# Optimization experiments

Hardware: AMD Instinct MI355X
Metric: run time of the kernel (lower is better)

The kernel has to match this reference:

```python
import jax, jax.numpy as jnp
import numpy as np

TEMPERATURE = 0.07
DELTA = 0.3
KA = 2.0
R = 3
B = 4096
D = 512
K = 4096
N = 131072
N_DICT_KEYS = 3  # len(cluster_result) dict: inst2cluster/centroids/density


def _l2norm(x):
    # torch F.normalize: x / max(||x||, 1e-12)
    return x / jnp.maximum(jnp.linalg.norm(x, axis=-1, keepdims=True), 1e-12)


def _inst_inst(anchor, pos):
    # CE with label 0 on [diag, off-diag] == logsumexp(full row) - diag
    a = _l2norm(anchor)
    p = _l2norm(pos)
    logits = (a @ p.T) / TEMPERATURE  # [B, B]
    return jax.nn.logsumexp(logits, axis=1) - jnp.diagonal(logits)


def _off_diag_idx(b):
    # row i -> column indices [0..b-1] excluding i (row-major boolean-mask order)
    j = jnp.arange(b - 1)[None, :]
    return j + (j >= jnp.arange(b)[:, None]).astype(jnp.int32)


def _inst_proto(anchor, i2c, centroids, density, index):
    b = anchor.shape[0]
    a = _l2norm(anchor)
    oidx = _off_diag_idx(b)
    loss = jnp.zeros(b, dtype=anchor.dtype)
    for r in range(R):
        protos = _l2norm(centroids[r])           # [K, D]
        pid = i2c[r][index]                       # [B]
        sim = a @ protos[pid].T                   # [B, B]
        diag = jnp.diagonal(sim)
        off = jnp.take_along_axis(sim, oidx, axis=1)  # [B, B-1]
        # faithful to original: divide concatenated logits column-wise by density[pid]
        logits = jnp.concatenate([diag[:, None], off], axis=1) / density[r][pid][None, :]
        loss = loss + (jax.nn.logsumexp(logits, axis=1) - logits[:, 0])
        loss = loss / N_DICT_KEYS  # original divides INSIDE the loop
    return loss


def _weights(audio, frame, a_i2c, a_cent, f_i2c, f_cent, index):
    fa = _l2norm(audio)
    ff = _l2norm(frame)
    rho = jnp.sum(fa * ff, axis=1)  # diagonal of fa @ ff.T
    for r in range(R):
        ca = a_cent[r][a_i2c[r][index]]  # [B, D] (NOT normalized, as in original)
        cf = f_cent[r][f_i2c[r][index]]
        rho = rho - jnp.sum(ca * cf, axis=1)  # diagonal of ca @ cf.T
    order = jnp.argsort(rho)
    sorted_rho = rho[order]
    mu = rho.mean() + DELTA * rho.std()
    sigma = rho.std() * jnp.sqrt(jnp.asarray(KA, rho.dtype))
    y = jnp.exp(-0.5 * ((sorted_rho - mu) / sigma) ** 2) / (jnp.sqrt(2.0 * jnp.pi) * sigma)
    y = jnp.cumsum(y)
    y = y / y[-1]
    w = y[jnp.argsort(order)]  # y at the rank of each rho_i
    return jax.lax.stop_gradient(w)  # original detaches via cpu().numpy()


def _forward(audio_emb, frame_emb, a_centroids, a_density, f_centroids, f_density,
             video_index, a_inst2cluster, f_inst2cluster):
    loss_v2f_ii = _inst_inst(audio_emb, frame_emb)
    loss_f2v_ii = _inst_inst(frame_emb, audio_emb)
    loss_v2f_ip = _inst_proto(audio_emb, f_inst2cluster, f_centroids, f_density, video_index)
    loss_f2v_ip = _inst_proto(frame_emb, a_inst2cluster, a_centroids, a_density, video_index)
    w = _weights(audio_emb, frame_emb, a_inst2cluster, a_centroids,
                 f_inst2cluster, f_centroids, video_index)
    loss_v2f = jnp.sum(w * (loss_v2f_ii + loss_v2f_ip)) / jnp.sum(w)
    loss_f2v = jnp.sum(w * (loss_f2v_ii + loss_f2v_ip)) / jnp.sum(w)
    return loss_v2f + loss_f2v


def setup_inputs() -> dict:
    key = jax.random.key(0)
    ks = jax.random.split(key, 9)
    return {
        "audio_emb": jax.random.normal(ks[0], (B, D), jnp.float32),
        "frame_emb": jax.random.normal(ks[1], (B, D), jnp.float32),
        "a_centroids": jax.random.normal(ks[2], (R, K, D), jnp.float32),
        "a_density": jax.random.uniform(ks[3], (R, K), jnp.float32, 0.3, 1.3),
        "f_centroids": jax.random.normal(ks[4], (R, K, D), jnp.float32),
        "f_density": jax.random.uniform(ks[5], (R, K), jnp.float32, 0.3, 1.3),
        "video_index": jax.random.randint(ks[6], (B,), 0, N),
        "a_inst2cluster": jax.random.randint(ks[7], (R, N), 0, K),
        "f_inst2cluster": jax.random.randint(ks[8], (R, N), 0, K),
    }


def reference(audio_emb, frame_emb, a_centroids, a_density, f_centroids, f_density,
              video_index, a_inst2cluster, f_inst2cluster):
    return _forward(audio_emb, frame_emb, a_centroids, a_density, f_centroids, f_density,
                    video_index, a_inst2cluster, f_inst2cluster)
```

## Files before the change

kernel.cpp:

```cpp
#include <hip/hip_runtime.h>
#include <math.h>

#define B 4096
#define D 512
#define KC 4096
#define NIDX 131072
#define RR 3
#define TEMP 0.07f
#define M_II 14.5f
#define M_IP 4.0f

typedef __bf16 bf16x8 __attribute__((ext_vector_type(8)));
typedef float f32x4 __attribute__((ext_vector_type(4)));

__device__ __forceinline__ void gload_lds16(const void* g, void* l) {
  __builtin_amdgcn_global_load_lds(
      (const __attribute__((address_space(1))) unsigned int*)g,
      (__attribute__((address_space(3))) unsigned int*)l, 16, 0, 0);
}

__device__ __forceinline__ float dot8(float4 a0, float4 a1, float4 b0, float4 b1) {
  return a0.x * b0.x + a0.y * b0.y + a0.z * b0.z + a0.w * b0.w
       + a1.x * b1.x + a1.y * b1.y + a1.z * b1.z + a1.w * b1.w;
}

__global__ __launch_bounds__(256) void prep_kernel(
    const float* __restrict__ audio, const float* __restrict__ frame,
    const float* __restrict__ a_cent, const float* __restrict__ a_dens,
    const float* __restrict__ f_cent, const float* __restrict__ f_dens,
    const int* __restrict__ vidx, const int* __restrict__ a_i2c,
    const int* __restrict__ f_i2c,
    __bf16* __restrict__ Xa, __bf16* __restrict__ Xf,
    __bf16* __restrict__ Yf, __bf16* __restrict__ Ya,
    float* __restrict__ invdd_f, float* __restrict__ invdd_a,
    float* __restrict__ rho0, float* __restrict__ pcp) {
  const int u = blockIdx.x * 4 + (threadIdx.x >> 6);
  const int lane = threadIdx.x & 63;

  if (u < 2 * B) {
    const float* src; __bf16* dst;
    if (u < B) { src = audio + (size_t)u * D; dst = Xa + (size_t)u * D; }
    else       { src = frame + (size_t)(u - B) * D; dst = Xf + (size_t)(u - B) * D; }
    const float4* s4 = (const float4*)src + lane * 2;
    float4 v0 = s4[0], v1 = s4[1];
    float ss = dot8(v0, v1, v0, v1);
    #pragma unroll
    for (int off = 32; off >= 1; off >>= 1) ss += __shfl_xor(ss, off, 64);
    float invn = 1.f / fmaxf(sqrtf(ss), 1e-12f);
    __bf16 o[8];
    o[0] = (__bf16)(v0.x * invn); o[1] = (__bf16)(v0.y * invn);
    o[2] = (__bf16)(v0.z * invn); o[3] = (__bf16)(v0.w * invn);
    o[4] = (__bf16)(v1.x * invn); o[5] = (__bf16)(v1.y * invn);
    o[6] = (__bf16)(v1.z * invn); o[7] = (__bf16)(v1.w * invn);
    *(bf16x8*)(dst + lane * 8) = *(bf16x8*)o;
  } else if (u < 5 * B) {
    const int q = u - 2 * B;
    const int r = q >> 12;
    const int j = q & (B - 1);
    const int idx = vidx[j];
    const int fp = f_i2c[r * NIDX + idx];
    const int ap = a_i2c[r * NIDX + idx];
    const float4* fr4 = (const float4*)(f_cent + ((size_t)r * KC + fp) * D) + lane * 2;
    const float4* ar4 = (const float4*)(a_cent + ((size_t)r * KC + ap) * D) + lane * 2;
    float4 f0 = fr4[0], f1 = fr4[1];
    float4 a0 = ar4[0], a1 = ar4[1];
    float sf = dot8(f0, f1, f0, f1);
    float sa = dot8(a0, a1, a0, a1);
    float pc = dot8(a0, a1, f0, f1);
    #pragma unroll
    for (int off = 32; off >= 1; off >>= 1) {
      sf += __shfl_xor(sf, off, 64);
      sa += __shfl_xor(sa, off, 64);
      pc += __shfl_xor(pc, off, 64);
    }
    float invnf = 1.f / fmaxf(sqrtf(sf), 1e-12f);
    float invna = 1.f / fmaxf(sqrtf(sa), 1e-12f);
    const int slot = r * B + j;
    __bf16 of[8], oa[8];
    of[0] = (__bf16)(f0.x * invnf); of[1] = (__bf16)(f0.y * invnf);
    of[2] = (__bf16)(f0.z * invnf); of[3] = (__bf16)(f0.w * invnf);
    of[4] = (__bf16)(f1.x * invnf); of[5] = (__bf16)(f1.y * invnf);
    of[6] = (__bf16)(f1.z * invnf); of[7] = (__bf16)(f1.w * invnf);
    oa[0] = (__bf16)(a0.x * invna); oa[1] = (__bf16)(a0.y * invna);
    oa[2] = (__bf16)(a0.z * invna); oa[3] = (__bf16)(a0.w * invna);
    oa[4] = (__bf16)(a1.x * invna); oa[5] = (__bf16)(a1.y * invna);
    oa[6] = (__bf16)(a1.z * invna); oa[7] = (__bf16)(a1.w * invna);
    *(bf16x8*)(Yf + (size_t)slot * D + lane * 8) = *(bf16x8*)of;
    *(bf16x8*)(Ya + (size_t)slot * D + lane * 8) = *(bf16x8*)oa;
    if (lane == 0) {
      invdd_f[slot] = 1.f / f_dens[(size_t)r * KC + fp];
      invdd_a[slot] = 1.f / a_dens[(size_t)r * KC + ap];
      pcp[slot] = pc;
    }
  } else {
    const int i = u - 5 * B;
    const float4* x4 = (const float4*)(audio + (size_t)i * D) + lane * 2;
    const float4* y4 = (const float4*)(frame + (size_t)i * D) + lane * 2;
    float4 a0 = x4[0], a1 = x4[1], f0 = y4[0], f1 = y4[1];
    float saf = dot8(a0, a1, f0, f1);
    float sa = dot8(a0, a1, a0, a1);
    float sf = dot8(f0, f1, f0, f1);
    #pragma unroll
    for (int off = 32; off >= 1; off >>= 1) {
      saf += __shfl_xor(saf, off, 64);
      sa  += __shfl_xor(sa, off, 64);
      sf  += __shfl_xor(sf, off, 64);
    }
    if (lane == 0)
      rho0[i] = saf / (fmaxf(sqrtf(sa), 1e-12f) * fmaxf(sqrtf(sf), 1e-12f));
  }
}

__global__ __launch_bounds__(512) void lse_mfma_kernel(
    const __bf16* __restrict__ Xa, const __bf16* __restrict__ Xf,
    const __bf16* __restrict__ Yf, const __bf16* __restrict__ Ya,
    const float* __restrict__ invdd_f, const float* __restrict__ invdd_a,
    float* __restrict__ sp, float* __restrict__ colsp,
    float* __restrict__ diagAll) {
  __shared__ __bf16 As[256 * 32];
  __shared__ __bf16 Bs[256 * 32];
  __shared__ float invL[260];
  __shared__ float part_s[4 * 256];
  __shared__ float colpart[2][256];

  const int b = blockIdx.x;
  const int xcd = b & 7;
  const int bi = b >> 3;
  const int slab = bi >> 4;
  const int w = bi & 15;
  const int gs = xcd * 14 + slab;
  const int yy = gs >> 4;
  const int s = gs & 15;
  const int bx = (s >> 2) * 4 + (w >> 2);
  const int bz = (s & 3) * 4 + (w & 3);

  const int job = (yy == 0) ? 0 : yy + 1;
  const int i0 = bx * 256;
  const int j0 = bz * 256;

  const __bf16* Ab; const __bf16* Bb; const float* invArr = nullptr;
  if (job == 0)      { Ab = Xa; Bb = Xf; }
  else if (job <= 4) { Ab = Xa; Bb = Yf + (size_t)(job - 2) * B * D;
                       invArr = invdd_f + (job - 2) * B; }
  else               { Ab = Xf; Bb = Ya + (size_t)(job - 5) * B * D;
                       invArr = invdd_a + (job - 5) * B; }
  const bool ii = (job == 0);
  const float invT = 1.f / TEMP;
  const float inv0 = ii ? invT : invArr[0];
  const float MJ = ii ? M_II : M_IP;

  const int tid = threadIdx.x;
  const int wv = tid >> 6;
  const int lane = tid & 63;
  const int wr = (wv >> 2) * 128;
  const int wc = (wv & 3) * 64;
  const int g = lane >> 4;
  const int cl = lane & 15;

  if (!ii && tid < 258) {
    int idx = j0 + tid; if (idx > B - 1) idx = B - 1;
    invL[tid] = invArr[idx];
  }

  const int srow = lane >> 2;
  const int skoff = (((lane & 3) ^ ((lane >> 3) & 3)) * 16);
  const int c0row = wv * 16 + srow;
  const char* gA0 = (const char*)Ab + (size_t)(i0 + c0row) * (D * 2) + skoff;
  const char* gA1 = gA0 + (size_t)128 * (D * 2);
  const char* gB0 = (const char*)Bb + (size_t)(j0 + c0row) * (D * 2) + skoff;
  const char* gB1 = gB0 + (size_t)128 * (D * 2);
  __bf16* lA0 = As + wv * 512;
  __bf16* lA1 = As + 4096 + wv * 512;
  __bf16* lB0 = Bs + wv * 512;
  __bf16* lB1 = Bs + 4096 + wv * 512;

  const int csw = (g ^ ((cl >> 1) & 3)) * 8;
  int aoff[8], boff[4];
  #pragma unroll
  for (int t = 0; t < 8; ++t) aoff[t] = (wr + t * 16 + cl) * 32 + csw;
  #pragma unroll
  for (int t = 0; t < 4; ++t) boff[t] = (wc + t * 16 + cl) * 32 + csw;

  f32x4 acc[8][4];
  #pragma unroll
  for (int ri = 0; ri < 8; ++ri)
    #pragma unroll
    for (int ci = 0; ci < 4; ++ci) acc[ri][ci] = (f32x4){0.f, 0.f, 0.f, 0.f};

  for (int kt = 0; kt < 16; ++kt) {
    __syncthreads();
    const int kb = kt * 64;
    gload_lds16(gA0 + kb, lA0);
    gload_lds16(gA1 + kb, lA1);
    gload_lds16(gB0 + kb, lB0);
    gload_lds16(gB1 + kb, lB1);
    __syncthreads();
    bf16x8 af[8], bfr[4];
    #pragma unroll
    for (int t = 0; t < 8; ++t) af[t] = *(const bf16x8*)(As + aoff[t]);
    #pragma unroll
    for (int t = 0; t < 4; ++t) bfr[t] = *(const bf16x8*)(Bs + boff[t]);
    #pragma unroll
    for (int ri = 0; ri < 8; ++ri)
      #pragma unroll
      for (int ci = 0; ci < 4; ++ci)
        acc[ri][ci] = __builtin_amdgcn_mfma_f32_16x16x32_bf16(
            af[ri], bfr[ci], acc[ri][ci], 0, 0, 0);
  }

  const bool dtile = (bx == bz);
  const int co = (j0 < i0) ? 1 : 0;
  float sacc[8][4];
  float csum[4] = {0.f, 0.f, 0.f, 0.f};
  #pragma unroll
  for (int ri = 0; ri < 8; ++ri) {
    #pragma unroll
    for (int v = 0; v < 4; ++v) {
      const int gi = i0 + wr + ri * 16 + g * 4 + v;
      float acc4 = 0.f;
      #pragma unroll
      for (int ci = 0; ci < 4; ++ci) {
        const int jloc = wc + ci * 16 + cl;
        const int gj = j0 + jloc;
        float sc;
        if (ii) sc = invT;
        else if (!dtile) sc = invL[jloc + co];
        else sc = (gj == gi) ? inv0 : invL[(gj < gi) ? (jloc + 1) : jloc];
        float lv = acc[ri][ci][v] * sc;
        if (dtile && gj == gi) diagAll[(size_t)job * B + gi] = lv;
        float ev = __expf(lv - MJ);
        acc4 += ev;
        if (ii) csum[ci] += ev;
      }
      sacc[ri][v] = acc4;
    }
  }
  if (ii) {
    #pragma unroll
    for (int ci = 0; ci < 4; ++ci) {
      csum[ci] += __shfl_xor(csum[ci], 16, 64);
      csum[ci] += __shfl_xor(csum[ci], 32, 64);
    }
    if (g == 0) {
      #pragma unroll
      for (int ci = 0; ci < 4; ++ci)
        colpart[wv >> 2][wc + ci * 16 + cl] = csum[ci];
    }
    __syncthreads();
    if (tid < 256)
      colsp[(size_t)bx * B + j0 + tid] =
          colpart[0][tid] + colpart[1][tid];
  }

  #pragma unroll
  for (int ri = 0; ri < 8; ++ri) {
    #pragma unroll
    for (int v = 0; v < 4; ++v) {
      float s2 = sacc[ri][v];
      #pragma unroll
      for (int off = 8; off >= 1; off >>= 1) s2 += __shfl_xor(s2, off, 64);
      if (cl == 0) part_s[(wv & 3) * 256 + wr + ri * 16 + g * 4 + v] = s2;
    }
  }
  __syncthreads();
  if (tid < 256) {
    size_t o = ((size_t)job * 16 + bz) * B + i0 + tid;
    sp[o] = part_s[tid] + part_s[256 + tid] + part_s[512 + tid] + part_s[768 + tid];
  }
}

__global__ __launch_bounds__(256) void merge_rank_kernel(
    const float* __restrict__ sp, const float* __restrict__ colsp,
    const float* __restrict__ diagAll, const float* __restrict__ rho0,
    const float* __restrict__ pcp,
    float* __restrict__ lossAll, int* __restrict__ rankArr,
    float* __restrict__ srho) {
  __shared__ float lr[B];
  __shared__ float cnt[256];
  const int blk = blockIdx.x;
  const int t = threadIdx.x;
  if (blk < 128) {
    int idx = blk * 256 + t;
    int job = idx >> 12;
    int i = idx & (B - 1);
    if (job == 1) {
      float stot = 0.f;
      #pragma unroll
      for (int x = 0; x < 16; ++x) stot += colsp[(size_t)x * B + i];
      lossAll[idx] = M_II + logf(stot) - diagAll[i];
    } else {
      const float* s16 = sp + (size_t)job * 16 * B + i;
      float stot = 0.f;
      #pragma unroll
      for (int x = 0; x < 16; ++x) stot += s16[(size_t)x * B];
      float MJ = (job < 2) ? M_II : M_IP;
      lossAll[idx] = MJ + logf(stot) - diagAll[(size_t)job * B + i];
    }
  } else {
    const int base = (blk - 128) * 32;
    const int il = t & 31;
    const int i = base + il;
    const int jlo = (t >> 5) * 512;
    for (int k = t; k < B; k += 256)
      lr[k] = rho0[k] - pcp[k] - pcp[B + k] - pcp[2 * B + k];
    __syncthreads();
    float my = lr[i];
    int rk = 0;
    #pragma unroll 8
    for (int j = jlo; j < jlo + 512; ++j) {
      float v = lr[j];
      rk += (v < my) || (v == my && j < i);
    }
    cnt[t] = (float)rk;
    __syncthreads();
    if (t < 32) {
      int r = 0;
      #pragma unroll
      for (int s = 0; s < 8; ++s) r += (int)cnt[s * 32 + t];
      rankArr[i] = r;
      srho[r] = my;
    }
  }
}

__global__ __launch_bounds__(1024) void cdf_final_kernel(
    const float* __restrict__ srho, const int* __restrict__ rankArr,
    const float* __restrict__ lossAll, float* __restrict__ out) {
  __shared__ float pdf[B];
  __shared__ float wred[16], wr1[16], wr2[16];
  __shared__ float wexc[16];
  __shared__ float mv[3];
  const int t = threadIdx.x;
  const int lane = t & 63;
  const int wid = t >> 6;

  float4 sv = *reinterpret_cast<const float4*>(srho + (size_t)t * 4);
  float s = sv.x + sv.y + sv.z + sv.w;
  #pragma unroll
  for (int off = 32; off >= 1; off >>= 1) s += __shfl_xor(s, off, 64);
  if (lane == 0) wred[wid] = s;
  __syncthreads();
  if (t == 0) {
    float tot = 0.f;
    #pragma unroll
    for (int w = 0; w < 16; ++w) tot += wred[w];
    mv[0] = tot / (float)B;
  }
  __syncthreads();
  const float mean = mv[0];
  __syncthreads();
  float dx = sv.x - mean, dy = sv.y - mean, dz = sv.z - mean, dw = sv.w - mean;
  float v = dx * dx + dy * dy + dz * dz + dw * dw;
  #pragma unroll
  for (int off = 32; off >= 1; off >>= 1) v += __shfl_xor(v, off, 64);
  if (lane == 0) wred[wid] = v;
  __syncthreads();
  if (t == 0) {
    float tot = 0.f;
    #pragma unroll
    for (int w = 0; w < 16; ++w) tot += wred[w];
    float sd = sqrtf(tot / (float)B);
    mv[0] = mean + 0.3f * sd;
    mv[1] = sd * 1.41421356237f;
  }
  __syncthreads();
  const float mu = mv[0], sg = mv[1];
  const float c = 1.f / (2.5066282746310002f * sg);
  float p[4];
  {
    float z0 = (sv.x - mu) / sg; p[0] = expf(-0.5f * z0 * z0) * c;
    float z1 = (sv.y - mu) / sg; p[1] = expf(-0.5f * z1 * z1) * c;
    float z2 = (sv.z - mu) / sg; p[2] = expf(-0.5f * z2 * z2) * c;
    float z3 = (sv.w - mu) / sg; p[3] = expf(-0.5f * z3 * z3) * c;
  }
  float chunk = p[0] + p[1] + p[2] + p[3];
  float incl = chunk;
  #pragma unroll
  for (int d = 1; d < 64; d <<= 1) {
    float n = __shfl_up(incl, d, 64);
    if (lane >= d) incl += n;
  }
  if (lane == 63) wred[wid] = incl;
  __syncthreads();
  if (t == 0) {
    float run = 0.f;
    #pragma unroll
    for (int w = 0; w < 16; ++w) { wexc[w] = run; run += wred[w]; }
    mv[2] = run;
  }
  __syncthreads();
  float run = wexc[wid] + (incl - chunk);
  #pragma unroll
  for (int e = 0; e < 4; ++e) { run += p[e]; pdf[t * 4 + e] = run; }
  const float ylast = mv[2];
  __syncthreads();
  int4 rks = *reinterpret_cast<const int4*>(rankArr + (size_t)t * 4);
  float sw = 0.f, s1 = 0.f, s2 = 0.f;
  #pragma unroll
  for (int e = 0; e < 4; ++e) {
    const int i = t * 4 + e;
    const int rk = (e == 0) ? rks.x : (e == 1) ? rks.y : (e == 2) ? rks.z : rks.w;
    float wi = pdf[rk] / ylast;
    float lpv = lossAll[2 * B + i] * (1.f / 27.f) + lossAll[3 * B + i] * (1.f / 9.f)
              + lossAll[4 * B + i] * (1.f / 3.f);
    float lpf = lossAll[5 * B + i] * (1.f / 27.f) + lossAll[6 * B + i] * (1.f / 9.f)
              + lossAll[7 * B + i] * (1.f / 3.f);
    sw += wi;
    s1 += wi * (lossAll[i] + lpv);
    s2 += wi * (lossAll[B + i] + lpf);
  }
  #pragma unroll
  for (int off = 32; off >= 1; off >>= 1) {
    sw += __shfl_xor(sw, off, 64);
    s1 += __shfl_xor(s1, off, 64);
    s2 += __shfl_xor(s2, off, 64);
  }
  if (lane == 0) { wred[wid] = sw; wr1[wid] = s1; wr2[wid] = s2; }
  __syncthreads();
  if (t == 0) {
    float tw = 0.f, t1 = 0.f, t2 = 0.f;
    #pragma unroll
    for (int w = 0; w < 16; ++w) { tw += wred[w]; t1 += wr1[w]; t2 += wr2[w]; }
    out[0] = t1 / tw + t2 / tw;
  }
}

extern "C" void kernel_launch(void* const* d_in, const int* in_sizes, int n_in,
                              void* d_out, int out_size, void* d_ws, size_t ws_size,
                              hipStream_t stream) {
  const float* audio  = (const float*)d_in[0];
  const float* frame  = (const float*)d_in[1];
  const float* a_cent = (const float*)d_in[2];
  const float* a_dens = (const float*)d_in[3];
  const float* f_cent = (const float*)d_in[4];
  const float* f_dens = (const float*)d_in[5];
  const int* vidx  = (const int*)d_in[6];
  const int* a_i2c = (const int*)d_in[7];
  const int* f_i2c = (const int*)d_in[8];
  float* out = (float*)d_out;

  const size_t BD = (size_t)B * D;
  char* base = (char*)d_ws;
  __bf16* Xa = (__bf16*)base;              base += BD * 2;
  __bf16* Xf = (__bf16*)base;              base += BD * 2;
  __bf16* Yf = (__bf16*)base;              base += 3 * BD * 2;
  __bf16* Ya = (__bf16*)base;              base += 3 * BD * 2;
  float* invdd_f = (float*)base;           base += 3 * B * 4;
  float* invdd_a = (float*)base;           base += 3 * B * 4;
  float* rho0    = (float*)base;           base += B * 4;
  float* pcp     = (float*)base;           base += 3 * B * 4;
  float* sp      = (float*)base;           base += 128 * B * 4;
  float* colsp   = (float*)base;           base += 16 * B * 4;
  float* diagAll = (float*)base;           base += 8 * B * 4;
  float* lossAll = (float*)base;           base += 8 * B * 4;
  float* srho    = (float*)base;           base += B * 4;
  int*   rankArr = (int*)base;

  prep_kernel<<<(6 * B) / 4, 256, 0, stream>>>(audio, frame, a_cent, a_dens,
                                               f_cent, f_dens, vidx, a_i2c, f_i2c,
                                               Xa, Xf, Yf, Ya, invdd_f, invdd_a,
                                               rho0, pcp);

  lse_mfma_kernel<<<1792, 512, 0, stream>>>(Xa, Xf, Yf, Ya, invdd_f, invdd_a,
                                            sp, colsp, diagAll);

  merge_rank_kernel<<<256, 256, 0, stream>>>(sp, colsp, diagAll, rho0, pcp,
                                             lossAll, rankArr, srho);
  cdf_final_kernel<<<1, 1024, 0, stream>>>(srho, rankArr, lossAll, out);
}
```

Baseline: 348.7 us.

## Triple-buffer LDS tiles with async prefetch two stages ahead in MFMA loop

Replaces the single-buffer load/sync/compute loop in the LSE MFMA kernel with a three-stage LDS ring. Global-to-LDS loads are issued two k-tiles ahead, and each iteration uses explicit vmcnt waits with one barrier instead of two __syncthreads. This is meant to hide global load latency behind the MFMA work. In exchange it triples the As/Bs shared memory, which can lower occupancy, and it depends on hand-written waitcnt counts being correct.

```diff
diff --git a/kernel.cpp b/kernel.cpp
--- a/kernel.cpp
+++ b/kernel.cpp
@@ -117,8 +117,8 @@
     const float* __restrict__ invdd_f, const float* __restrict__ invdd_a,
     float* __restrict__ sp, float* __restrict__ colsp,
     float* __restrict__ diagAll) {
-  __shared__ __bf16 As[256 * 32];
-  __shared__ __bf16 Bs[256 * 32];
+  __shared__ __bf16 As[3 * 256 * 32];
+  __shared__ __bf16 Bs[3 * 256 * 32];
   __shared__ float invL[260];
   __shared__ float part_s[4 * 256];
   __shared__ float colpart[2][256];
@@ -161,6 +161,7 @@
     int idx = j0 + tid; if (idx > B - 1) idx = B - 1;
     invL[tid] = invArr[idx];
   }
+  asm volatile("s_waitcnt vmcnt(0)" ::: "memory");
 
   const int srow = lane >> 2;
   const int skoff = (((lane & 3) ^ ((lane >> 3) & 3)) * 16);
@@ -187,25 +188,42 @@
     #pragma unroll
     for (int ci = 0; ci < 4; ++ci) acc[ri][ci] = (f32x4){0.f, 0.f, 0.f, 0.f};
 
+  gload_lds16(gA0, lA0);
+  gload_lds16(gA1, lA1);
+  gload_lds16(gB0, lB0);
+  gload_lds16(gB1, lB1);
+  gload_lds16(gA0 + 64, lA0 + 8192);
+  gload_lds16(gA1 + 64, lA1 + 8192);
+  gload_lds16(gB0 + 64, lB0 + 8192);
+  gload_lds16(gB1 + 64, lB1 + 8192);
+
+  int cur = 0;
+  int stg = 16384;
+  #pragma unroll 1
   for (int kt = 0; kt < 16; ++kt) {
-    __syncthreads();
-    const int kb = kt * 64;
-    gload_lds16(gA0 + kb, lA0);
-    gload_lds16(gA1 + kb, lA1);
-    gload_lds16(gB0 + kb, lB0);
-    gload_lds16(gB1 + kb, lB1);
-    __syncthreads();
+    if (kt == 15) asm volatile("s_waitcnt vmcnt(0)" ::: "memory");
+    else          asm volatile("s_waitcnt vmcnt(4)" ::: "memory");
+    asm volatile("s_barrier" ::: "memory");
+    if (kt <= 13) {
+      const int kb = (kt + 2) * 64;
+      gload_lds16(gA0 + kb, lA0 + stg);
+      gload_lds16(gA1 + kb, lA1 + stg);
+      gload_lds16(gB0 + kb, lB0 + stg);
+      gload_lds16(gB1 + kb, lB1 + stg);
+    }
     bf16x8 af[8], bfr[4];
     #pragma unroll
-    for (int t = 0; t < 8; ++t) af[t] = *(const bf16x8*)(As + aoff[t]);
-    #pragma unroll
-    for (int t = 0; t < 4; ++t) bfr[t] = *(const bf16x8*)(Bs + boff[t]);
+    for (int t = 0; t < 8; ++t) af[t] = *(const bf16x8*)(As + cur + aoff[t]);
+    #pragma unroll
+    for (int t = 0; t < 4; ++t) bfr[t] = *(const bf16x8*)(Bs + cur + boff[t]);
     #pragma unroll
     for (int ri = 0; ri < 8; ++ri)
       #pragma unroll
       for (int ci = 0; ci < 4; ++ci)
         acc[ri][ci] = __builtin_amdgcn_mfma_f32_16x16x32_bf16(
             af[ri], bfr[ci], acc[ri][ci], 0, 0, 0);
+    cur = (cur == 16384) ? 0 : cur + 8192;
+    stg = (stg == 16384) ? 0 : stg + 8192;
   }
 
   const bool dtile = (bx == bz);
```

Result: no change. 345.2 us (-1.0%).

## Double-buffer LDS tiles with K=128 stages, interleaved loads and exp2 epilogue

Applied to the files above, without the earlier changes.

Reworks the GEMM main loop of the LSE kernel. It now uses double-buffered LDS tiles of 128-wide K chunks, and the global-to-LDS loads for the next stage are interleaved with four MFMA sub-phases, coordinated by explicit vmcnt waits, barriers and s_setprio. This is meant to hide global load latency behind matrix math instead of syncing twice per 64-wide K step. It also folds log2(e) into the scale factors so the epilogue uses exp2f instead of __expf, and rescales diagonal values by ln2. LDS use grows fourfold, which may lower occupancy.

```diff
diff --git a/kernel.cpp b/kernel.cpp
--- a/kernel.cpp
+++ b/kernel.cpp
@@ -9,6 +9,8 @@
 #define TEMP 0.07f
 #define M_II 14.5f
 #define M_IP 4.0f
+#define LOG2E 1.44269504f
+#define LN2 0.69314718f
 
 typedef __bf16 bf16x8 __attribute__((ext_vector_type(8)));
 typedef float f32x4 __attribute__((ext_vector_type(4)));
@@ -88,8 +90,8 @@
     *(bf16x8*)(Yf + (size_t)slot * D + lane * 8) = *(bf16x8*)of;
     *(bf16x8*)(Ya + (size_t)slot * D + lane * 8) = *(bf16x8*)oa;
     if (lane == 0) {
-      invdd_f[slot] = 1.f / f_dens[(size_t)r * KC + fp];
-      invdd_a[slot] = 1.f / a_dens[(size_t)r * KC + ap];
+      invdd_f[slot] = LOG2E / f_dens[(size_t)r * KC + fp];
+      invdd_a[slot] = LOG2E / a_dens[(size_t)r * KC + ap];
       pcp[slot] = pc;
     }
   } else {
@@ -117,8 +119,8 @@
     const float* __restrict__ invdd_f, const float* __restrict__ invdd_a,
     float* __restrict__ sp, float* __restrict__ colsp,
     float* __restrict__ diagAll) {
-  __shared__ __bf16 As[256 * 32];
-  __shared__ __bf16 Bs[256 * 32];
+  __shared__ __bf16 As[2 * 16384];
+  __shared__ __bf16 Bs[2 * 16384];
   __shared__ float invL[260];
   __shared__ float part_s[4 * 256];
   __shared__ float colpart[2][256];
@@ -145,9 +147,9 @@
   else               { Ab = Xf; Bb = Ya + (size_t)(job - 5) * B * D;
                        invArr = invdd_a + (job - 5) * B; }
   const bool ii = (job == 0);
-  const float invT = 1.f / TEMP;
-  const float inv0 = ii ? invT : invArr[0];
-  const float MJ = ii ? M_II : M_IP;
+  const float invT2 = (1.f / TEMP) * LOG2E;
+  const float inv0 = ii ? invT2 : invArr[0];
+  const float M2 = (ii ? M_II : M_IP) * LOG2E;
 
   const int tid = threadIdx.x;
   const int wv = tid >> 6;
@@ -161,18 +163,12 @@
     int idx = j0 + tid; if (idx > B - 1) idx = B - 1;
     invL[tid] = invArr[idx];
   }
+  asm volatile("s_waitcnt vmcnt(0)" ::: "memory");
 
   const int srow = lane >> 2;
   const int skoff = (((lane & 3) ^ ((lane >> 3) & 3)) * 16);
-  const int c0row = wv * 16 + srow;
-  const char* gA0 = (const char*)Ab + (size_t)(i0 + c0row) * (D * 2) + skoff;
-  const char* gA1 = gA0 + (size_t)128 * (D * 2);
-  const char* gB0 = (const char*)Bb + (size_t)(j0 + c0row) * (D * 2) + skoff;
-  const char* gB1 = gB0 + (size_t)128 * (D * 2);
-  __bf16* lA0 = As + wv * 512;
-  __bf16* lA1 = As + 4096 + wv * 512;
-  __bf16* lB0 = Bs + wv * 512;
-  __bf16* lB1 = Bs + 4096 + wv * 512;
+  const char* gA = (const char*)Ab + (size_t)(i0 + wv * 16 + srow) * 1024 + skoff;
+  const char* gB = (const char*)Bb + (size_t)(j0 + wv * 16 + srow) * 1024 + skoff;
 
   const int csw = (g ^ ((cl >> 1) & 3)) * 8;
   int aoff[8], boff[4];
@@ -187,25 +183,92 @@
     #pragma unroll
     for (int ci = 0; ci < 4; ++ci) acc[ri][ci] = (f32x4){0.f, 0.f, 0.f, 0.f};
 
-  for (int kt = 0; kt < 16; ++kt) {
-    __syncthreads();
-    const int kb = kt * 64;
-    gload_lds16(gA0 + kb, lA0);
-    gload_lds16(gA1 + kb, lA1);
-    gload_lds16(gB0 + kb, lB0);
-    gload_lds16(gB1 + kb, lB1);
-    __syncthreads();
-    bf16x8 af[8], bfr[4];
-    #pragma unroll
-    for (int t = 0; t < 8; ++t) af[t] = *(const bf16x8*)(As + aoff[t]);
-    #pragma unroll
-    for (int t = 0; t < 4; ++t) bfr[t] = *(const bf16x8*)(Bs + boff[t]);
-    #pragma unroll
-    for (int ri = 0; ri < 8; ++ri)
-      #pragma unroll
-      for (int ci = 0; ci < 4; ++ci)
-        acc[ri][ci] = __builtin_amdgcn_mfma_f32_16x16x32_bf16(
-            af[ri], bfr[ci], acc[ri][ci], 0, 0, 0);
+  #pragma unroll
+  for (int h = 0; h < 2; ++h) {
+    gload_lds16(gA + h * 131072,      As + h * 4096 + wv * 512);
+    gload_lds16(gA + h * 131072 + 64, As + 8192 + h * 4096 + wv * 512);
+    gload_lds16(gB + h * 131072,      Bs + h * 4096 + wv * 512);
+    gload_lds16(gB + h * 131072 + 64, Bs + 8192 + h * 4096 + wv * 512);
+  }
+
+  bf16x8 bfr[4], afr[4];
+  #pragma unroll 1
+  for (int kt = 0; kt < 8; ++kt) {
+    const int bo = (kt & 1) * 16384;
+    const int nb = 16384 - bo;
+    const int kb = (kt + 1) * 128;
+    const bool more = (kt < 7);
+    if (more) {
+      gload_lds16(gA + kb,          As + nb + wv * 512);
+      gload_lds16(gA + 131072 + kb, As + nb + 4096 + wv * 512);
+    }
+    if (kt == 7) asm volatile("s_waitcnt vmcnt(0)" ::: "memory");
+    else         asm volatile("s_waitcnt vmcnt(2)" ::: "memory");
+    asm volatile("s_barrier" ::: "memory");
+    #pragma unroll
+    for (int c = 0; c < 4; ++c) bfr[c] = *(const bf16x8*)(Bs + bo + boff[c]);
+    #pragma unroll
+    for (int i = 0; i < 4; ++i) afr[i] = *(const bf16x8*)(As + bo + aoff[i]);
+    asm volatile("s_barrier" ::: "memory");
+    __builtin_amdgcn_s_setprio(1);
+    #pragma unroll
+    for (int i = 0; i < 4; ++i)
+      #pragma unroll
+      for (int c = 0; c < 4; ++c)
+        acc[i][c] = __builtin_amdgcn_mfma_f32_16x16x32_bf16(
+            afr[i], bfr[c], acc[i][c], 0, 0, 0);
+    __builtin_amdgcn_s_setprio(0);
+    asm volatile("s_barrier" ::: "memory");
+    if (more) {
+      gload_lds16(gA + 64 + kb,          As + nb + 8192 + wv * 512);
+      gload_lds16(gA + 131072 + 64 + kb, As + nb + 12288 + wv * 512);
+    }
+    #pragma unroll
+    for (int i = 0; i < 4; ++i) afr[i] = *(const bf16x8*)(As + bo + aoff[4 + i]);
+    asm volatile("s_barrier" ::: "memory");
+    __builtin_amdgcn_s_setprio(1);
+    #pragma unroll
+    for (int i = 0; i < 4; ++i)
+      #pragma unroll
+      for (int c = 0; c < 4; ++c)
+        acc[4 + i][c] = __builtin_amdgcn_mfma_f32_16x16x32_bf16(
+            afr[i], bfr[c], acc[4 + i][c], 0, 0, 0);
+    __builtin_amdgcn_s_setprio(0);
+    asm volatile("s_barrier" ::: "memory");
+    if (more) {
+      gload_lds16(gB + kb,          Bs + nb + wv * 512);
+      gload_lds16(gB + 131072 + kb, Bs + nb + 4096 + wv * 512);
+    }
+    #pragma unroll
+    for (int c = 0; c < 4; ++c) bfr[c] = *(const bf16x8*)(Bs + bo + 8192 + boff[c]);
+    #pragma unroll
+    for (int i = 0; i < 4; ++i) afr[i] = *(const bf16x8*)(As + bo + 8192 + aoff[i]);
+    asm volatile("s_barrier" ::: "memory");
+    __builtin_amdgcn_s_setprio(1);
+    #pragma unroll
+    for (int i = 0; i < 4; ++i)
+      #pragma unroll
+      for (int c = 0; c < 4; ++c)
+        acc[i][c] = __builtin_amdgcn_mfma_f32_16x16x32_bf16(
+            afr[i], bfr[c], acc[i][c], 0, 0, 0);
+    __builtin_amdgcn_s_setprio(0);
+    asm volatile("s_barrier" ::: "memory");
+    if (more) {
+      gload_lds16(gB + 64 + kb,          Bs + nb + 8192 + wv * 512);
+      gload_lds16(gB + 131072 + 64 + kb, Bs + nb + 12288 + wv * 512);
+    }
+    #pragma unroll
+    for (int i = 0; i < 4; ++i) afr[i] = *(const bf16x8*)(As + bo + 8192 + aoff[4 + i]);
+    asm volatile("s_barrier" ::: "memory");
+    __builtin_amdgcn_s_setprio(1);
+    #pragma unroll
+    for (int i = 0; i < 4; ++i)
+      #pragma unroll
+      for (int c = 0; c < 4; ++c)
+        acc[4 + i][c] = __builtin_amdgcn_mfma_f32_16x16x32_bf16(
+            afr[i], bfr[c], acc[4 + i][c], 0, 0, 0);
+    __builtin_amdgcn_s_setprio(0);
+    asm volatile("s_barrier" ::: "memory");
   }
 
   const bool dtile = (bx == bz);
@@ -223,12 +286,12 @@
         const int jloc = wc + ci * 16 + cl;
         const int gj = j0 + jloc;
         float sc;
-        if (ii) sc = invT;
+        if (ii) sc = invT2;
         else if (!dtile) sc = invL[jloc + co];
         else sc = (gj == gi) ? inv0 : invL[(gj < gi) ? (jloc + 1) : jloc];
-        float lv = acc[ri][ci][v] * sc;
-        if (dtile && gj == gi) diagAll[(size_t)job * B + gi] = lv;
-        float ev = __expf(lv - MJ);
+        float lv2 = acc[ri][ci][v] * sc;
+        if (dtile && gj == gi) diagAll[(size_t)job * B + gi] = lv2 * LN2;
+        float ev = exp2f(lv2 - M2);
         acc4 += ev;
         if (ii) csum[ci] += ev;
       }
```

Measured after the change: 365.7 us. 4.9% more time.
